# Kernel tuning notes

Measured on AMD Instinct MI355X. Metric: run time of the kernel, lower is better.

Reference implementation:

```python
import jax, jax.numpy as jnp
import numpy as np

B, N, L, C = 16, 2048, 12, 32  # batch, num_nodes, seq_len, channels


def setup_inputs() -> dict:
    key = jax.random.key(0)
    k1, k2, k3 = jax.random.split(key, 3)
    x = jax.random.normal(k1, (B, N, L, C), dtype=jnp.float32)
    # memory parameter: xavier_uniform over (channels, num_nodes)
    limit = float(np.sqrt(6.0 / (C + N)))
    memory = jax.random.uniform(k2, (C, N), minval=-limit, maxval=limit, dtype=jnp.float32)
    # nn.Linear(2, 1): weight (1, 2), bias (1,)
    fc_limit = float(np.sqrt(1.0 / 2.0))
    fc_w = jax.random.uniform(k3, (1, 2), minval=-fc_limit, maxval=fc_limit, dtype=jnp.float32)
    fc_b = jnp.zeros((1,), dtype=jnp.float32)
    return {"x": x, "memory": memory, "fc_w": fc_w, "fc_b": fc_b}


def reference(x, memory, fc_w, fc_b):
    # x: (B, N, L, C) -> permute to (B, C, N, L) as in the torch module
    xp = jnp.transpose(x, (0, 3, 1, 2))
    scale = 1.0 / float(np.sqrt(xp.shape[1]))  # 1/sqrt(channels)
    # adj_dyn_1: einsum over channel+time with memory -> (B, N, N)
    a1 = jax.nn.softmax(jax.nn.relu(jnp.einsum('bcnl,cm->bnm', xp, memory) * scale), axis=-1)
    # adj_dyn_2: time-summed node features gram matrix -> (B, N, N)
    xs = xp.sum(-1)  # (B, C, N)
    a2 = jax.nn.softmax(jax.nn.relu(jnp.einsum('bcn,bcm->bnm', xs, xs) * scale), axis=-1)
    # fc over the stacked pair: Linear(2,1) == w0*a1 + w1*a2 + b
    adj = a1 * fc_w[0, 0] + a2 * fc_w[0, 1] + fc_b[0]  # (B, N, N)
    k = int(adj.shape[1] * 0.8)
    _, idx = jax.lax.top_k(adj, k)  # idx: (B, N, k)
    b_ix = jnp.arange(adj.shape[0])[:, None, None]
    n_ix = jnp.arange(adj.shape[1])[None, :, None]
    mask = jnp.zeros_like(adj).at[b_ix, n_ix, idx].set(1.0)
    return jax.nn.softmax(adj * mask, axis=-1)
```

## Files before the change

### kernel.cpp

```cpp
#include <hip/hip_runtime.h>
#include <hip/hip_bf16.h>
#include <cstdint>
#include <cstddef>

#define B_ 16
#define N_ 2048
#define L_ 12
#define C_ 32
#define KTOP 1638
#define SCALE 0.17677669529663687f
#define LOG2E 1.44269504088896f

typedef __attribute__((ext_vector_type(8))) short short8v;
typedef __attribute__((ext_vector_type(4))) float f32x4;

#if __has_builtin(__builtin_amdgcn_exp2f)
#define EXP2F(x) __builtin_amdgcn_exp2f(x)
#else
#define EXP2F(x) exp2f(x)
#endif

__device__ __forceinline__ unsigned short bf16_rne(float v) {
  unsigned u = __float_as_uint(v);
  u += 0x7FFFu + ((u >> 16) & 1u);
  return (unsigned short)(u >> 16);
}
__device__ __forceinline__ unsigned key15(unsigned short b16) {
  const unsigned s = b16 >> 15;
  return ((((unsigned)b16) ^ 0x8000u ^ (s * 0x7FFFu)) >> 1) & 0x7FFFu;
}
__device__ __forceinline__ float exp_poly4(float x) {
  return fmaf(x, fmaf(x, fmaf(x, fmaf(x, 0.041666667f, 0.166666667f), 0.5f), 1.f), 1.f);
}

__global__ __launch_bounds__(256) void prep_kernel(const float* __restrict__ x,
                                                   const float* __restrict__ mem,
                                                   unsigned short* __restrict__ xsH,
                                                   unsigned short* __restrict__ xsL,
                                                   unsigned short* __restrict__ memT) {
  const int b = blockIdx.y, n0 = blockIdx.x * 64;
  const int c = threadIdx.x & 31, nr = threadIdx.x >> 5;
#pragma unroll
  for (int i = 0; i < 8; ++i) {
    const int n = n0 + i * 8 + nr;
    const float* px = x + ((size_t)(b * N_ + n) * L_) * C_ + c;
    float s = 0.f;
#pragma unroll
    for (int l = 0; l < L_; ++l) s += px[l * C_];
    const unsigned short h = bf16_rne(s);
    const float hf = __uint_as_float((unsigned)h << 16);
    const unsigned short lo = bf16_rne(s - hf);
    const size_t o = (size_t)(b * N_ + n) * C_ + c;
    xsH[o] = h;
    xsL[o] = lo;
  }
  if (b == 0) {
#pragma unroll
    for (int i = 0; i < 8; ++i) {
      const int idx = i * 256 + threadIdx.x;
      const int ml = idx >> 5, cc = idx & 31;
      memT[(size_t)(n0 + ml) * C_ + cc] = bf16_rne(mem[(size_t)cc * N_ + n0 + ml]);
    }
  }
}

__global__ __launch_bounds__(512, 4) void adj_kernel(
    const unsigned short* __restrict__ xsH, const unsigned short* __restrict__ xsL,
    const unsigned short* __restrict__ memT, const float* __restrict__ fc_w,
    const float* __restrict__ fc_b, float* __restrict__ out) {
  __shared__ unsigned pbuf[8][2049];
  __shared__ float red1[8][8], red2[8][8];

  const int tid = threadIdx.x, wid = tid >> 6, lane = tid & 63;
  const int l15 = lane & 15, g = lane >> 4;
  const int b = blockIdx.y, n0 = blockIdx.x * 8;

  const int fr = (l15 < 8) ? l15 : ((l15 - 6) & 7);
  const int rbase = (g & 1) * 4 + (g & 2);
  const int g8 = g * 8;
  const size_t arow = (size_t)(b * N_ + n0 + fr) * C_ + g8;
  const short8v hiA = *(const short8v*)(xsH + arow);
  const short8v loFA = *(const short8v*)(xsL + arow);

  const f32x4 zero = {0.f, 0.f, 0.f, 0.f};
  const float K = SCALE * LOG2E;
  const float C2 = -80.f * LOG2E;
  const int mbase = wid * 256 + l15;
  const size_t bcol = (size_t)b * N_ * C_ + (size_t)mbase * C_ + g8;
  const unsigned short* pH = xsH + bcol;
  const unsigned short* pL = xsL + bcol;
  const unsigned short* pM = memT + (size_t)mbase * C_ + g8;
  unsigned* pw = &pbuf[rbase][mbase];

  float s1[2] = {0.f, 0.f}, s2[2] = {0.f, 0.f};

#pragma unroll
  for (int t = 0; t < 16; ++t) {
    const short8v hiB = *(const short8v*)(pH + t * (16 * C_));
    const short8v loB = *(const short8v*)(pL + t * (16 * C_));
    const short8v mB  = *(const short8v*)(pM + t * (16 * C_));

    f32x4 acc1 = __builtin_amdgcn_mfma_f32_16x16x32_bf16(hiA, mB, zero, 0, 0, 0);
    f32x4 acc2 = __builtin_amdgcn_mfma_f32_16x16x32_bf16(hiA, hiB, zero, 0, 0, 0);
    acc2 = __builtin_amdgcn_mfma_f32_16x16x32_bf16(hiA, loB, acc2, 0, 0, 0);
    acc2 = __builtin_amdgcn_mfma_f32_16x16x32_bf16(loFA, hiB, acc2, 0, 0, 0);

#pragma unroll
    for (int s = 0; s < 2; ++s) {
      const float p1 = EXP2F(fmaxf(acc1[s], 0.f) * K);
      const float p2 = EXP2F(fminf(fmaf(fmaxf(acc2[s], 0.f), K, C2), 127.f));
      s1[s] += p1; s2[s] += p2;
      union { __hip_bfloat162 h2; unsigned u; } pk;
      pk.h2 = __float22bfloat162_rn(float2{p1, p2});
      pw[s * 2049 + t * 16] = pk.u;
    }
  }

#pragma unroll
  for (int d = 1; d < 16; d <<= 1) {
#pragma unroll
    for (int s = 0; s < 2; ++s) {
      s1[s] += __shfl_xor(s1[s], d);
      s2[s] += __shfl_xor(s2[s], d);
    }
  }
  if (l15 == 0) {
#pragma unroll
    for (int s = 0; s < 2; ++s) {
      red1[wid][rbase + s] = s1[s];
      red2[wid][rbase + s] = s2[s];
    }
  }
  __syncthreads();

  const int r = wid;
  float S1 = 0.f, S2 = 0.f;
#pragma unroll
  for (int w = 0; w < 8; ++w) { S1 += red1[w][r]; S2 += red2[w][r]; }
  const float w0 = fc_w[0], w1 = fc_w[1], bb = fc_b[0];
  const float i1 = w0 / S1, i2 = w1 / S2;
  const unsigned* prow = &pbuf[0][0] + r * 2049;

  const float p2t = __uint_as_float((unsigned)bf16_rne(EXP2F(C2)) << 16);
  const float T = fmaf(p2t, i2, fmaf(1.0f, i1, bb));

  unsigned exb[16];
  float ssum = 0.f;
  unsigned cge = 0, cgt = 0;
#pragma unroll
  for (int k = 0; k < 8; ++k) {
    const uint4 q = *(const uint4*)&prow[4 * lane + 256 * k];
    const unsigned qq[4] = {q.x, q.y, q.z, q.w};
    float e4[4];
#pragma unroll
    for (int c4 = 0; c4 < 4; ++c4) {
      const float p1 = __uint_as_float(qq[c4] << 16);
      const float p2 = __uint_as_float(qq[c4] & 0xFFFF0000u);
      const float adj = fmaf(p2, i2, fmaf(p1, i1, bb));
      cge += (adj >= T) ? 1u : 0u;
      cgt += (adj >  T) ? 1u : 0u;
      const float am = (adj >= T) ? adj : 0.f;
      const float e = exp_poly4(am);
      e4[c4] = e;
      ssum += e;
    }
    union { __hip_bfloat162 h2; unsigned u; } pa, pb2;
    pa.h2  = __float22bfloat162_rn(float2{e4[0], e4[1]});
    pb2.h2 = __float22bfloat162_rn(float2{e4[2], e4[3]});
    exb[2 * k] = pa.u; exb[2 * k + 1] = pb2.u;
  }
  unsigned comb = cge | (cgt << 16);
#pragma unroll
  for (int d = 1; d < 64; d <<= 1) {
    comb += (unsigned)__shfl_xor((int)comb, d);
    ssum += __shfl_xor(ssum, d);
  }
  const unsigned CGE = comb & 0xFFFFu, CGT = comb >> 16;

  float* op = out + ((size_t)(b * N_ + n0 + r)) * N_;

  if (CGE >= KTOP && CGT < KTOP) {
    const float inv = 1.f / ssum;
#pragma unroll
    for (int k = 0; k < 8; ++k) {
      float4 o;
      o.x = __uint_as_float(exb[2 * k] << 16) * inv;
      o.y = __uint_as_float(exb[2 * k] & 0xFFFF0000u) * inv;
      o.z = __uint_as_float(exb[2 * k + 1] << 16) * inv;
      o.w = __uint_as_float(exb[2 * k + 1] & 0xFFFF0000u) * inv;
      *(float4*)(op + 4 * lane + 256 * k) = o;
    }
  } else {
    unsigned pk2[16], kg[16];
#pragma unroll
    for (int k = 0; k < 8; ++k) {
      const uint4 q = *(const uint4*)&prow[4 * lane + 256 * k];
      const unsigned qq[4] = {q.x, q.y, q.z, q.w};
      float a4[4];
#pragma unroll
      for (int c4 = 0; c4 < 4; ++c4) {
        const float p1 = __uint_as_float(qq[c4] << 16);
        const float p2 = __uint_as_float(qq[c4] & 0xFFFF0000u);
        a4[c4] = fmaf(p2, i2, fmaf(p1, i1, bb));
      }
      union { __hip_bfloat162 h2; unsigned u; } cA, cB;
      cA.h2 = __float22bfloat162_rn(float2{a4[0], a4[1]});
      cB.h2 = __float22bfloat162_rn(float2{a4[2], a4[3]});
      pk2[2 * k] = cA.u; pk2[2 * k + 1] = cB.u;
      unsigned sgn = (cA.u >> 15) & 0x00010001u;
      unsigned srt = cA.u ^ 0x80008000u ^ (sgn * 0x7FFFu);
      kg[2 * k] = ((srt >> 1) & 0x7FFF7FFFu) | 0x80008000u;
      sgn = (pk2[2 * k + 1] >> 15) & 0x00010001u;
      srt = pk2[2 * k + 1] ^ 0x80008000u ^ (sgn * 0x7FFFu);
      kg[2 * k + 1] = ((srt >> 1) & 0x7FFF7FFFu) | 0x80008000u;
    }
    unsigned mn = 0x7FFFu, mx = 0u;
#pragma unroll
    for (int j = 0; j < 16; ++j) {
      const unsigned k15 = kg[j] & 0x7FFF7FFFu;
      mn = min(mn, min(k15 & 0xFFFFu, k15 >> 16));
      mx = max(mx, max(k15 & 0xFFFFu, k15 >> 16));
    }
#pragma unroll
    for (int d = 1; d < 64; d <<= 1) {
      mn = min(mn, (unsigned)__shfl_xor((int)mn, d));
      mx = max(mx, (unsigned)__shfl_xor((int)mx, d));
    }
    unsigned lo2 = mn, hi2 = mx;
#pragma unroll 1
    for (int it = 0; it < 15; ++it) {
      if (lo2 >= hi2) break;
      const unsigned mid = (lo2 + hi2 + 1u) >> 1;
      const unsigned mm = mid * 0x10001u;
      unsigned c0 = 0;
#pragma unroll
      for (int j = 0; j < 16; ++j) c0 += ((kg[j] - mm) >> 15) & 0x10001u;
      unsigned cnt = (c0 & 0xFFFFu) + (c0 >> 16);
#pragma unroll
      for (int d = 1; d < 64; d <<= 1) cnt += (unsigned)__shfl_xor((int)cnt, d);
      if (cnt >= KTOP) lo2 = mid; else hi2 = mid - 1u;
    }
    const unsigned lolo = lo2 * 0x10001u;
    float s2sum = 0.f;
    float exf[32];
#pragma unroll
    for (int j = 0; j < 16; ++j) {
      const unsigned ge = kg[j] - lolo;
      const float aA = (ge & 0x8000u) ? __uint_as_float(pk2[j] << 16) : 0.f;
      const float aB = (ge & 0x80000000u) ? __uint_as_float(pk2[j] & 0xFFFF0000u) : 0.f;
      const float eA = EXP2F(aA * LOG2E);
      const float eB = EXP2F(aB * LOG2E);
      exf[2 * j] = eA; exf[2 * j + 1] = eB;
      s2sum += eA + eB;
    }
#pragma unroll
    for (int d = 1; d < 64; d <<= 1) s2sum += __shfl_xor(s2sum, d);
    const float inv = 1.f / s2sum;
#pragma unroll
    for (int k = 0; k < 8; ++k) {
      float4 o;
      o.x = exf[4 * k + 0] * inv; o.y = exf[4 * k + 1] * inv;
      o.z = exf[4 * k + 2] * inv; o.w = exf[4 * k + 3] * inv;
      *(float4*)(op + 4 * lane + 256 * k) = o;
    }
  }
}

extern "C" void kernel_launch(void* const* d_in, const int* in_sizes, int n_in,
                              void* d_out, int out_size, void* d_ws, size_t ws_size,
                              hipStream_t stream) {
  const float* x   = (const float*)d_in[0];
  const float* mem = (const float*)d_in[1];
  const float* fcw = (const float*)d_in[2];
  const float* fcb = (const float*)d_in[3];
  float* out = (float*)d_out;
  unsigned short* xsH  = (unsigned short*)d_ws;
  unsigned short* xsL  = xsH + (size_t)B_ * N_ * C_;
  unsigned short* memT = xsL + (size_t)B_ * N_ * C_;

  dim3 g1(N_ / 64, B_);
  prep_kernel<<<g1, 256, 0, stream>>>(x, mem, xsH, xsL, memT);
  dim3 g2(N_ / 8, B_);
  adj_kernel<<<g2, 512, 0, stream>>>(xsH, xsL, memT, fcw, fcb, out);
}
```

Baseline: 133.3 us.

## Keep per-row probabilities in registers for fast path, recompute into LDS on fallback

```diff
diff --git a/kernel.cpp b/kernel.cpp
--- a/kernel.cpp
+++ b/kernel.cpp
@@ -25,10 +25,6 @@
   u += 0x7FFFu + ((u >> 16) & 1u);
   return (unsigned short)(u >> 16);
 }
-__device__ __forceinline__ unsigned key15(unsigned short b16) {
-  const unsigned s = b16 >> 15;
-  return ((((unsigned)b16) ^ 0x8000u ^ (s * 0x7FFFu)) >> 1) & 0x7FFFu;
-}
 __device__ __forceinline__ float exp_poly4(float x) {
   return fmaf(x, fmaf(x, fmaf(x, fmaf(x, 0.041666667f, 0.166666667f), 0.5f), 1.f), 1.f);
 }
@@ -70,6 +66,8 @@
     const float* __restrict__ fc_b, float* __restrict__ out) {
   __shared__ unsigned pbuf[8][2049];
   __shared__ float red1[8][8], red2[8][8];
+  __shared__ unsigned redC[8][8];
+  __shared__ float redE[8][8];
 
   const int tid = threadIdx.x, wid = tid >> 6, lane = tid & 63;
   const int l15 = lane & 15, g = lane >> 4;
@@ -90,9 +88,9 @@
   const unsigned short* pH = xsH + bcol;
   const unsigned short* pL = xsL + bcol;
   const unsigned short* pM = memT + (size_t)mbase * C_ + g8;
-  unsigned* pw = &pbuf[rbase][mbase];
 
   float s1[2] = {0.f, 0.f}, s2[2] = {0.f, 0.f};
+  unsigned pA[16], pB[16];
 
 #pragma unroll
   for (int t = 0; t < 16; ++t) {
@@ -105,14 +103,21 @@
     acc2 = __builtin_amdgcn_mfma_f32_16x16x32_bf16(hiA, loB, acc2, 0, 0, 0);
     acc2 = __builtin_amdgcn_mfma_f32_16x16x32_bf16(loFA, hiB, acc2, 0, 0, 0);
 
-#pragma unroll
-    for (int s = 0; s < 2; ++s) {
-      const float p1 = EXP2F(fmaxf(acc1[s], 0.f) * K);
-      const float p2 = EXP2F(fminf(fmaf(fmaxf(acc2[s], 0.f), K, C2), 127.f));
-      s1[s] += p1; s2[s] += p2;
+    {
+      const float p1 = EXP2F(fmaxf(acc1[0], 0.f) * K);
+      const float p2 = EXP2F(fminf(fmaf(fmaxf(acc2[0], 0.f), K, C2), 127.f));
+      s1[0] += p1; s2[0] += p2;
       union { __hip_bfloat162 h2; unsigned u; } pk;
       pk.h2 = __float22bfloat162_rn(float2{p1, p2});
-      pw[s * 2049 + t * 16] = pk.u;
+      pA[t] = pk.u;
+    }
+    {
+      const float p1 = EXP2F(fmaxf(acc1[1], 0.f) * K);
+      const float p2 = EXP2F(fminf(fmaf(fmaxf(acc2[1], 0.f), K, C2), 127.f));
+      s1[1] += p1; s2[1] += p2;
+      union { __hip_bfloat162 h2; unsigned u; } pk;
+      pk.h2 = __float22bfloat162_rn(float2{p1, p2});
+      pB[t] = pk.u;
     }
   }
 
@@ -125,72 +130,103 @@
     }
   }
   if (l15 == 0) {
-#pragma unroll
-    for (int s = 0; s < 2; ++s) {
-      red1[wid][rbase + s] = s1[s];
-      red2[wid][rbase + s] = s2[s];
-    }
+    red1[rbase][wid] = s1[0]; red1[rbase + 1][wid] = s1[1];
+    red2[rbase][wid] = s2[0]; red2[rbase + 1][wid] = s2[1];
   }
   __syncthreads();
-
-  const int r = wid;
-  float S1 = 0.f, S2 = 0.f;
-#pragma unroll
-  for (int w = 0; w < 8; ++w) { S1 += red1[w][r]; S2 += red2[w][r]; }
+  float S1A = 0.f, S1B = 0.f, S2A = 0.f, S2B = 0.f;
+#pragma unroll
+  for (int w = 0; w < 8; ++w) {
+    S1A += red1[rbase][w]; S1B += red1[rbase + 1][w];
+    S2A += red2[rbase][w]; S2B += red2[rbase + 1][w];
+  }
   const float w0 = fc_w[0], w1 = fc_w[1], bb = fc_b[0];
-  const float i1 = w0 / S1, i2 = w1 / S2;
-  const unsigned* prow = &pbuf[0][0] + r * 2049;
+  const float i1A = w0 / S1A, i2A = w1 / S2A;
+  const float i1B = w0 / S1B, i2B = w1 / S2B;
 
   const float p2t = __uint_as_float((unsigned)bf16_rne(EXP2F(C2)) << 16);
-  const float T = fmaf(p2t, i2, fmaf(1.0f, i1, bb));
-
-  unsigned exb[16];
-  float ssum = 0.f;
-  unsigned cge = 0, cgt = 0;
-#pragma unroll
-  for (int k = 0; k < 8; ++k) {
-    const uint4 q = *(const uint4*)&prow[4 * lane + 256 * k];
-    const unsigned qq[4] = {q.x, q.y, q.z, q.w};
-    float e4[4];
-#pragma unroll
-    for (int c4 = 0; c4 < 4; ++c4) {
-      const float p1 = __uint_as_float(qq[c4] << 16);
-      const float p2 = __uint_as_float(qq[c4] & 0xFFFF0000u);
-      const float adj = fmaf(p2, i2, fmaf(p1, i1, bb));
-      cge += (adj >= T) ? 1u : 0u;
-      cgt += (adj >  T) ? 1u : 0u;
-      const float am = (adj >= T) ? adj : 0.f;
-      const float e = exp_poly4(am);
-      e4[c4] = e;
-      ssum += e;
-    }
-    union { __hip_bfloat162 h2; unsigned u; } pa, pb2;
-    pa.h2  = __float22bfloat162_rn(float2{e4[0], e4[1]});
-    pb2.h2 = __float22bfloat162_rn(float2{e4[2], e4[3]});
-    exb[2 * k] = pa.u; exb[2 * k + 1] = pb2.u;
-  }
-  unsigned comb = cge | (cgt << 16);
-#pragma unroll
-  for (int d = 1; d < 64; d <<= 1) {
-    comb += (unsigned)__shfl_xor((int)comb, d);
-    ssum += __shfl_xor(ssum, d);
-  }
-  const unsigned CGE = comb & 0xFFFFu, CGT = comb >> 16;
-
-  float* op = out + ((size_t)(b * N_ + n0 + r)) * N_;
-
-  if (CGE >= KTOP && CGT < KTOP) {
-    const float inv = 1.f / ssum;
-#pragma unroll
-    for (int k = 0; k < 8; ++k) {
-      float4 o;
-      o.x = __uint_as_float(exb[2 * k] << 16) * inv;
-      o.y = __uint_as_float(exb[2 * k] & 0xFFFF0000u) * inv;
-      o.z = __uint_as_float(exb[2 * k + 1] << 16) * inv;
-      o.w = __uint_as_float(exb[2 * k + 1] & 0xFFFF0000u) * inv;
-      *(float4*)(op + 4 * lane + 256 * k) = o;
+  const float TA = fmaf(p2t, i2A, fmaf(1.0f, i1A, bb));
+  const float TB = fmaf(p2t, i2B, fmaf(1.0f, i1B, bb));
+
+  unsigned cntA = 0, cntB = 0;
+  float ssA = 0.f, ssB = 0.f;
+#pragma unroll
+  for (int t = 0; t < 16; ++t) {
+    const unsigned qa = pA[t], qb = pB[t];
+    const float adjA = fmaf(__uint_as_float(qa & 0xFFFF0000u), i2A,
+                      fmaf(__uint_as_float(qa << 16), i1A, bb));
+    const float adjB = fmaf(__uint_as_float(qb & 0xFFFF0000u), i2B,
+                      fmaf(__uint_as_float(qb << 16), i1B, bb));
+    cntA += ((adjA >= TA) ? 1u : 0u) + ((adjA > TA) ? 0x10000u : 0u);
+    cntB += ((adjB >= TB) ? 1u : 0u) + ((adjB > TB) ? 0x10000u : 0u);
+    const float eA = exp_poly4((adjA >= TA) ? adjA : 0.f);
+    const float eB = exp_poly4((adjB >= TB) ? adjB : 0.f);
+    ssA += eA; ssB += eB;
+    union { __hip_bfloat162 h2; unsigned u; } pk;
+    pk.h2 = __float22bfloat162_rn(float2{eA, eB});
+    pA[t] = pk.u;
+  }
+
+#pragma unroll
+  for (int d = 1; d < 16; d <<= 1) {
+    cntA += (unsigned)__shfl_xor((int)cntA, d);
+    cntB += (unsigned)__shfl_xor((int)cntB, d);
+    ssA += __shfl_xor(ssA, d);
+    ssB += __shfl_xor(ssB, d);
+  }
+  if (l15 == 0) {
+    redC[rbase][wid] = cntA; redC[rbase + 1][wid] = cntB;
+    redE[rbase][wid] = ssA;  redE[rbase + 1][wid] = ssB;
+  }
+  __syncthreads();
+  unsigned CA = 0, CB = 0;
+  float SEA = 0.f, SEB = 0.f;
+#pragma unroll
+  for (int w = 0; w < 8; ++w) {
+    CA += redC[rbase][w]; CB += redC[rbase + 1][w];
+    SEA += redE[rbase][w]; SEB += redE[rbase + 1][w];
+  }
+  const bool okA = ((CA & 0xFFFFu) >= KTOP) && ((CA >> 16) < KTOP);
+  const bool okB = ((CB & 0xFFFFu) >= KTOP) && ((CB >> 16) < KTOP);
+
+  if (__all(okA && okB)) {
+    const float invA = 1.f / SEA, invB = 1.f / SEB;
+    float* opA = out + ((size_t)(b * N_ + n0 + rbase)) * N_ + mbase;
+    float* opB = opA + N_;
+#pragma unroll
+    for (int t = 0; t < 16; ++t) {
+      opA[t * 16] = __uint_as_float(pA[t] << 16) * invA;
+      opB[t * 16] = __uint_as_float(pA[t] & 0xFFFF0000u) * invB;
     }
   } else {
+    unsigned* pw = &pbuf[rbase][mbase];
+#pragma unroll 2
+    for (int t = 0; t < 16; ++t) {
+      const short8v hiB = *(const short8v*)(pH + t * (16 * C_));
+      const short8v loB = *(const short8v*)(pL + t * (16 * C_));
+      const short8v mB  = *(const short8v*)(pM + t * (16 * C_));
+      f32x4 acc1 = __builtin_amdgcn_mfma_f32_16x16x32_bf16(hiA, mB, zero, 0, 0, 0);
+      f32x4 acc2 = __builtin_amdgcn_mfma_f32_16x16x32_bf16(hiA, hiB, zero, 0, 0, 0);
+      acc2 = __builtin_amdgcn_mfma_f32_16x16x32_bf16(hiA, loB, acc2, 0, 0, 0);
+      acc2 = __builtin_amdgcn_mfma_f32_16x16x32_bf16(loFA, hiB, acc2, 0, 0, 0);
+#pragma unroll
+      for (int s = 0; s < 2; ++s) {
+        const float p1 = EXP2F(fmaxf(acc1[s], 0.f) * K);
+        const float p2 = EXP2F(fminf(fmaf(fmaxf(acc2[s], 0.f), K, C2), 127.f));
+        union { __hip_bfloat162 h2; unsigned u; } pk;
+        pk.h2 = __float22bfloat162_rn(float2{p1, p2});
+        pw[s * 2049 + t * 16] = pk.u;
+      }
+    }
+    __syncthreads();
+
+    const int r = wid;
+    float S1w = 0.f, S2w = 0.f;
+#pragma unroll
+    for (int w = 0; w < 8; ++w) { S1w += red1[r][w]; S2w += red2[r][w]; }
+    const float i1 = w0 / S1w, i2 = w1 / S2w;
+    const unsigned* prow = &pbuf[0][0] + r * 2049;
+
     unsigned pk2[16], kg[16];
 #pragma unroll
     for (int k = 0; k < 8; ++k) {
@@ -203,15 +239,15 @@
         const float p2 = __uint_as_float(qq[c4] & 0xFFFF0000u);
         a4[c4] = fmaf(p2, i2, fmaf(p1, i1, bb));
       }
-      union { __hip_bfloat162 h2; unsigned u; } cA, cB;
-      cA.h2 = __float22bfloat162_rn(float2{a4[0], a4[1]});
-      cB.h2 = __float22bfloat162_rn(float2{a4[2], a4[3]});
-      pk2[2 * k] = cA.u; pk2[2 * k + 1] = cB.u;
-      unsigned sgn = (cA.u >> 15) & 0x00010001u;
-      unsigned srt = cA.u ^ 0x80008000u ^ (sgn * 0x7FFFu);
+      union { __hip_bfloat162 h2; unsigned u; } cA2, cB2;
+      cA2.h2 = __float22bfloat162_rn(float2{a4[0], a4[1]});
+      cB2.h2 = __float22bfloat162_rn(float2{a4[2], a4[3]});
+      pk2[2 * k] = cA2.u; pk2[2 * k + 1] = cB2.u;
+      unsigned sgn = (cA2.u >> 15) & 0x00010001u;
+      unsigned srt = cA2.u ^ 0x80008000u ^ (sgn * 0x7FFFu);
       kg[2 * k] = ((srt >> 1) & 0x7FFF7FFFu) | 0x80008000u;
-      sgn = (pk2[2 * k + 1] >> 15) & 0x00010001u;
-      srt = pk2[2 * k + 1] ^ 0x80008000u ^ (sgn * 0x7FFFu);
+      sgn = (cB2.u >> 15) & 0x00010001u;
+      srt = cB2.u ^ 0x80008000u ^ (sgn * 0x7FFFu);
       kg[2 * k + 1] = ((srt >> 1) & 0x7FFF7FFFu) | 0x80008000u;
     }
     unsigned mn = 0x7FFFu, mx = 0u;
@@ -256,6 +292,7 @@
 #pragma unroll
     for (int d = 1; d < 64; d <<= 1) s2sum += __shfl_xor(s2sum, d);
     const float inv = 1.f / s2sum;
+    float* op = out + ((size_t)(b * N_ + n0 + r)) * N_;
 #pragma unroll
     for (int k = 0; k < 8; ++k) {
       float4 o;
```

Result: slower. 142.2 us (+6.6%).

## Process 16 rows per block to fill MFMA tiles and fold scale into memory

Applied to the files above, without the earlier changes.

```diff
diff --git a/kernel.cpp b/kernel.cpp
--- a/kernel.cpp
+++ b/kernel.cpp
@@ -10,6 +10,7 @@
 #define KTOP 1638
 #define SCALE 0.17677669529663687f
 #define LOG2E 1.44269504088896f
+#define PITCH 2064
 
 typedef __attribute__((ext_vector_type(8))) short short8v;
 typedef __attribute__((ext_vector_type(4))) float f32x4;
@@ -24,10 +25,6 @@
   unsigned u = __float_as_uint(v);
   u += 0x7FFFu + ((u >> 16) & 1u);
   return (unsigned short)(u >> 16);
-}
-__device__ __forceinline__ unsigned key15(unsigned short b16) {
-  const unsigned s = b16 >> 15;
-  return ((((unsigned)b16) ^ 0x8000u ^ (s * 0x7FFFu)) >> 1) & 0x7FFFu;
 }
 __device__ __forceinline__ float exp_poly4(float x) {
   return fmaf(x, fmaf(x, fmaf(x, fmaf(x, 0.041666667f, 0.166666667f), 0.5f), 1.f), 1.f);
@@ -55,47 +52,47 @@
     xsL[o] = lo;
   }
   if (b == 0) {
+    const float KF = SCALE * LOG2E;
 #pragma unroll
     for (int i = 0; i < 8; ++i) {
       const int idx = i * 256 + threadIdx.x;
       const int ml = idx >> 5, cc = idx & 31;
-      memT[(size_t)(n0 + ml) * C_ + cc] = bf16_rne(mem[(size_t)cc * N_ + n0 + ml]);
-    }
-  }
-}
-
-__global__ __launch_bounds__(512, 4) void adj_kernel(
+      memT[(size_t)(n0 + ml) * C_ + cc] = bf16_rne(mem[(size_t)cc * N_ + n0 + ml] * KF);
+    }
+  }
+}
+
+__global__ __launch_bounds__(1024, 4) void adj_kernel(
     const unsigned short* __restrict__ xsH, const unsigned short* __restrict__ xsL,
     const unsigned short* __restrict__ memT, const float* __restrict__ fc_w,
     const float* __restrict__ fc_b, float* __restrict__ out) {
-  __shared__ unsigned pbuf[8][2049];
-  __shared__ float red1[8][8], red2[8][8];
+  __shared__ unsigned pbuf[16][PITCH];
+  __shared__ float red1[16][16], red2[16][16];
+  __shared__ unsigned okfl[16];
 
   const int tid = threadIdx.x, wid = tid >> 6, lane = tid & 63;
   const int l15 = lane & 15, g = lane >> 4;
-  const int b = blockIdx.y, n0 = blockIdx.x * 8;
-
-  const int fr = (l15 < 8) ? l15 : ((l15 - 6) & 7);
-  const int rbase = (g & 1) * 4 + (g & 2);
+  const int b = blockIdx.y, n0 = blockIdx.x * 16;
+
   const int g8 = g * 8;
-  const size_t arow = (size_t)(b * N_ + n0 + fr) * C_ + g8;
+  const size_t arow = (size_t)(b * N_ + n0 + l15) * C_ + g8;
   const short8v hiA = *(const short8v*)(xsH + arow);
   const short8v loFA = *(const short8v*)(xsL + arow);
 
   const f32x4 zero = {0.f, 0.f, 0.f, 0.f};
   const float K = SCALE * LOG2E;
   const float C2 = -80.f * LOG2E;
-  const int mbase = wid * 256 + l15;
+  const int mbase = wid * 128 + l15;
   const size_t bcol = (size_t)b * N_ * C_ + (size_t)mbase * C_ + g8;
   const unsigned short* pH = xsH + bcol;
   const unsigned short* pL = xsL + bcol;
   const unsigned short* pM = memT + (size_t)mbase * C_ + g8;
-  unsigned* pw = &pbuf[rbase][mbase];
-
-  float s1[2] = {0.f, 0.f}, s2[2] = {0.f, 0.f};
-
-#pragma unroll
-  for (int t = 0; t < 16; ++t) {
+  unsigned* pw = &pbuf[g * 4][mbase];
+
+  float s1[4] = {0.f, 0.f, 0.f, 0.f}, s2[4] = {0.f, 0.f, 0.f, 0.f};
+
+#pragma unroll
+  for (int t = 0; t < 8; ++t) {
     const short8v hiB = *(const short8v*)(pH + t * (16 * C_));
     const short8v loB = *(const short8v*)(pL + t * (16 * C_));
     const short8v mB  = *(const short8v*)(pM + t * (16 * C_));
@@ -106,29 +103,29 @@
     acc2 = __builtin_amdgcn_mfma_f32_16x16x32_bf16(loFA, hiB, acc2, 0, 0, 0);
 
 #pragma unroll
-    for (int s = 0; s < 2; ++s) {
-      const float p1 = EXP2F(fmaxf(acc1[s], 0.f) * K);
-      const float p2 = EXP2F(fminf(fmaf(fmaxf(acc2[s], 0.f), K, C2), 127.f));
-      s1[s] += p1; s2[s] += p2;
+    for (int j = 0; j < 4; ++j) {
+      const float p1 = EXP2F(fmaxf(acc1[j], 0.f));
+      const float p2 = EXP2F(fminf(fmaf(fmaxf(acc2[j], 0.f), K, C2), 127.f));
+      s1[j] += p1; s2[j] += p2;
       union { __hip_bfloat162 h2; unsigned u; } pk;
       pk.h2 = __float22bfloat162_rn(float2{p1, p2});
-      pw[s * 2049 + t * 16] = pk.u;
+      pw[j * PITCH + t * 16] = pk.u;
     }
   }
 
 #pragma unroll
   for (int d = 1; d < 16; d <<= 1) {
 #pragma unroll
-    for (int s = 0; s < 2; ++s) {
-      s1[s] += __shfl_xor(s1[s], d);
-      s2[s] += __shfl_xor(s2[s], d);
+    for (int j = 0; j < 4; ++j) {
+      s1[j] += __shfl_xor(s1[j], d);
+      s2[j] += __shfl_xor(s2[j], d);
     }
   }
   if (l15 == 0) {
 #pragma unroll
-    for (int s = 0; s < 2; ++s) {
-      red1[wid][rbase + s] = s1[s];
-      red2[wid][rbase + s] = s2[s];
+    for (int j = 0; j < 4; ++j) {
+      red1[g * 4 + j][wid] = s1[j];
+      red2[g * 4 + j][wid] = s2[j];
     }
   }
   __syncthreads();
@@ -136,10 +133,10 @@
   const int r = wid;
   float S1 = 0.f, S2 = 0.f;
 #pragma unroll
-  for (int w = 0; w < 8; ++w) { S1 += red1[w][r]; S2 += red2[w][r]; }
+  for (int w = 0; w < 16; ++w) { S1 += red1[r][w]; S2 += red2[r][w]; }
   const float w0 = fc_w[0], w1 = fc_w[1], bb = fc_b[0];
   const float i1 = w0 / S1, i2 = w1 / S2;
-  const unsigned* prow = &pbuf[0][0] + r * 2049;
+  const unsigned* prow = &pbuf[0][0] + r * PITCH;
 
   const float p2t = __uint_as_float((unsigned)bf16_rne(EXP2F(C2)) << 16);
   const float T = fmaf(p2t, i2, fmaf(1.0f, i1, bb));
@@ -159,8 +156,7 @@
       const float adj = fmaf(p2, i2, fmaf(p1, i1, bb));
       cge += (adj >= T) ? 1u : 0u;
       cgt += (adj >  T) ? 1u : 0u;
-      const float am = (adj >= T) ? adj : 0.f;
-      const float e = exp_poly4(am);
+      const float e = exp_poly4((adj >= T) ? adj : 0.f);
       e4[c4] = e;
       ssum += e;
     }
@@ -176,10 +172,17 @@
     ssum += __shfl_xor(ssum, d);
   }
   const unsigned CGE = comb & 0xFFFFu, CGT = comb >> 16;
+  const bool ok = (CGE >= KTOP) && (CGT < KTOP);
+
+  if (lane == 0) okfl[wid] = ok ? 1u : 0u;
+  __syncthreads();
+  unsigned allok = 1u;
+#pragma unroll
+  for (int w = 0; w < 16; ++w) allok &= okfl[w];
 
   float* op = out + ((size_t)(b * N_ + n0 + r)) * N_;
 
-  if (CGE >= KTOP && CGT < KTOP) {
+  if (allok) {
     const float inv = 1.f / ssum;
 #pragma unroll
     for (int k = 0; k < 8; ++k) {
@@ -191,6 +194,7 @@
       *(float4*)(op + 4 * lane + 256 * k) = o;
     }
   } else {
+    const float i1f = i1, i2f = i2;
     unsigned pk2[16], kg[16];
 #pragma unroll
     for (int k = 0; k < 8; ++k) {
@@ -201,17 +205,17 @@
       for (int c4 = 0; c4 < 4; ++c4) {
         const float p1 = __uint_as_float(qq[c4] << 16);
         const float p2 = __uint_as_float(qq[c4] & 0xFFFF0000u);
-        a4[c4] = fmaf(p2, i2, fmaf(p1, i1, bb));
+        a4[c4] = fmaf(p2, i2f, fmaf(p1, i1f, bb));
       }
-      union { __hip_bfloat162 h2; unsigned u; } cA, cB;
-      cA.h2 = __float22bfloat162_rn(float2{a4[0], a4[1]});
-      cB.h2 = __float22bfloat162_rn(float2{a4[2], a4[3]});
-      pk2[2 * k] = cA.u; pk2[2 * k + 1] = cB.u;
-      unsigned sgn = (cA.u >> 15) & 0x00010001u;
-      unsigned srt = cA.u ^ 0x80008000u ^ (sgn * 0x7FFFu);
+      union { __hip_bfloat162 h2; unsigned u; } cA2, cB2;
+      cA2.h2 = __float22bfloat162_rn(float2{a4[0], a4[1]});
+      cB2.h2 = __float22bfloat162_rn(float2{a4[2], a4[3]});
+      pk2[2 * k] = cA2.u; pk2[2 * k + 1] = cB2.u;
+      unsigned sgn = (cA2.u >> 15) & 0x00010001u;
+      unsigned srt = cA2.u ^ 0x80008000u ^ (sgn * 0x7FFFu);
       kg[2 * k] = ((srt >> 1) & 0x7FFF7FFFu) | 0x80008000u;
-      sgn = (pk2[2 * k + 1] >> 15) & 0x00010001u;
-      srt = pk2[2 * k + 1] ^ 0x80008000u ^ (sgn * 0x7FFFu);
+      sgn = (cB2.u >> 15) & 0x00010001u;
+      srt = cB2.u ^ 0x80008000u ^ (sgn * 0x7FFFu);
       kg[2 * k + 1] = ((srt >> 1) & 0x7FFF7FFFu) | 0x80008000u;
     }
     unsigned mn = 0x7FFFu, mx = 0u;
@@ -280,6 +284,6 @@
 
   dim3 g1(N_ / 64, B_);
   prep_kernel<<<g1, 256, 0, stream>>>(x, mem, xsH, xsL, memT);
-  dim3 g2(N_ / 8, B_);
-  adj_kernel<<<g2, 512, 0, stream>>>(xsH, xsL, memT, fcw, fcb, out);
-}
+  dim3 g2(N_ / 16, B_);
+  adj_kernel<<<g2, 1024, 0, stream>>>(xsH, xsL, memT, fcw, fcb, out);
+}
```

New measurement: 136.1 us. 2.1% more time.
